# Kernel optimization log

Hardware: AMD Instinct MI355X
Metric: run time of the kernel (lower is better)

The kernel has to match this reference:

```python
import jax, jax.numpy as jnp
import numpy as np

INPUT_BITS = 1024   # window size
N_STATE = 2048      # state-layer neurons
N_OUT = 256         # output-layer neurons
NB_S = 16           # bits per state neuron
NB_O = 16           # bits per output neuron
HASH = 65536        # RAM table size per neuron (2**16 -> hash == direct address)
T = 64              # number of windows (65536 / 1024)


def _addresses(bits, conn, nbits):
    # bits: [n_in] int32 in {0,1}; conn: [N, nbits] int32 indices into bits
    pow2 = (jnp.int32(1) << jnp.arange(nbits, dtype=jnp.int32))  # [nbits]
    gathered = bits[conn]                                        # [N, nbits]
    return (gathered * pow2).sum(axis=-1) % HASH                 # [N]


def setup_inputs() -> dict:
    key = jax.random.key(0)
    k1, k2, k3, k4, k5 = jax.random.split(key, 5)
    input_bits = jax.random.randint(k1, (1, T * INPUT_BITS), 0, 2, dtype=jnp.int32)
    conn_state = jax.random.randint(k2, (N_STATE, NB_S), 0, INPUT_BITS + N_STATE, dtype=jnp.int32)
    conn_out = jax.random.randint(k3, (N_OUT, NB_O), 0, N_STATE, dtype=jnp.int32)
    # RAM lookup tables (learned contents), float so cell values are differentiable
    state_table = jax.random.uniform(k4, (N_STATE, HASH), dtype=jnp.float32)
    output_table = jax.random.uniform(k5, (N_OUT, HASH), dtype=jnp.float32)
    return {
        "input_bits": input_bits,
        "conn_state": conn_state,
        "conn_out": conn_out,
        "state_table": state_table,
        "output_table": output_table,
    }


def reference(input_bits, conn_state, conn_out, state_table, output_table):
    # make_windows: [1, T*INPUT_BITS] -> T windows of [INPUT_BITS]
    windows = input_bits.reshape(T, INPUT_BITS)

    def step(state_bits, window):
        # state_layer_input = cat([window_bits, state_bits])  -> [INPUT_BITS + N_STATE]
        x = jnp.concatenate([window, state_bits])
        addr = _addresses(x, conn_state, NB_S)                           # [N_STATE]
        vals = jnp.take_along_axis(state_table, addr[:, None], axis=1)[:, 0]
        new_state = (vals > 0.5).astype(jnp.int32)  # detach/clone: state is discrete bits
        return new_state, None

    state0 = jnp.zeros((N_STATE,), dtype=jnp.int32)  # _reset_state: all zeros
    final_state, _ = jax.lax.scan(step, state0, windows)

    # output layer on final state (only the last step's output is returned)
    addr = _addresses(final_state, conn_out, NB_O)                       # [N_OUT]
    out = jnp.take_along_axis(output_table, addr[:, None], axis=1)[:, 0]
    return out[None, :]  # [1, N_OUT] raw table reads (decoder thresholds these)
```

## Files before the change

### kernel.cpp

```cpp
#include <hip/hip_runtime.h>

#define T_STEPS 64
#define INPUT_BITS 1024
#define N_STATE 2048
#define N_OUT 256
#define NB 16
#define HASHROW 65536
#define NBLK 32

#define WS_CNT  0
#define WS_BUF0 8
#define WS_BUF1 72
#define WS_PK   192
#define WS_WORDS_NEEDED 2240

__global__ __launch_bounds__(256) void ram_init_kernel(
    const int* __restrict__ input_bits, unsigned int* __restrict__ ws)
{
    const int tid = threadIdx.x, lane = tid & 63;
    const int gw = blockIdx.x * 4 + (tid >> 6);
#pragma unroll
    for (int i = 0; i < 8; i++) {
        int g = gw * 8 + i;
        int v = input_bits[g * 64 + lane];
        unsigned long long m = __ballot(v != 0);
        if (lane == 0) {
            ws[WS_PK + 2 * g]     = (unsigned int)(m & 0xFFFFFFFFull);
            ws[WS_PK + 2 * g + 1] = (unsigned int)(m >> 32);
        }
    }
    if (blockIdx.x == 0 && tid < 192) ws[tid] = 0u;
}

__global__ __launch_bounds__(256) void ram_main_kernel(
    const int* __restrict__ conn_state,
    const int* __restrict__ conn_out,
    const float* __restrict__ state_table,
    const float* __restrict__ output_table,
    unsigned int* __restrict__ ws,
    float* __restrict__ out)
{
    __shared__ unsigned int pk[2048];
    __shared__ unsigned int xw[96];

    const int tid = threadIdx.x, lane = tid & 63, wave = tid >> 6;
    const int b = blockIdx.x;

    for (int i = tid; i < 2048; i += 256) pk[i] = ws[WS_PK + i];

    const unsigned int neuron = (unsigned int)(b * 64 + lane);
    int cn[NB];
#pragma unroll
    for (int j = 0; j < NB; j++) cn[j] = conn_state[neuron * NB + j];
    const float* row = state_table + (size_t)neuron * HASHROW;

    if (wave == 0) xw[32 + lane] = 0u;
    __syncthreads();
    if (wave == 0 && lane < 32) xw[lane] = pk[lane];
    __syncthreads();

    unsigned int* const buf0 = ws + WS_BUF0;
    unsigned int* const buf1 = ws + WS_BUF1;
    unsigned int* const cnt  = ws + WS_CNT;

    for (int t = 0; t < T_STEPS; t++) {
        unsigned int* const bw = ((t + 1) & 1) ? buf1 : buf0;
        if (wave == 0) {
            unsigned int a = 0;
#pragma unroll
            for (int j = 0; j < NB; j++)
                a |= ((xw[cn[j] >> 5] >> (cn[j] & 31)) & 1u) << j;
            float v = row[a];
            unsigned long long m = __ballot(v > 0.5f);
            if (lane == 0) {
                __hip_atomic_store(&bw[2 * b],     (unsigned int)(m & 0xFFFFFFFFull),
                                   __ATOMIC_RELAXED, __HIP_MEMORY_SCOPE_AGENT);
                __hip_atomic_store(&bw[2 * b + 1], (unsigned int)(m >> 32),
                                   __ATOMIC_RELAXED, __HIP_MEMORY_SCOPE_AGENT);
            }
        }
        __syncthreads();
        if (tid == 0) {
            __hip_atomic_fetch_add(cnt, 1u, __ATOMIC_ACQ_REL, __HIP_MEMORY_SCOPE_AGENT);
            const unsigned int target = (unsigned int)(NBLK * (t + 1));
            while (__hip_atomic_load(cnt, __ATOMIC_ACQUIRE, __HIP_MEMORY_SCOPE_AGENT) < target)
                __builtin_amdgcn_s_sleep(1);
        }
        __syncthreads();
        if (wave == 0) {
            unsigned int s = __hip_atomic_load(&bw[lane], __ATOMIC_RELAXED,
                                               __HIP_MEMORY_SCOPE_AGENT);
            xw[32 + lane] = s;
            if (t < T_STEPS - 1 && lane < 32) xw[lane] = pk[(t + 1) * 32 + lane];
        }
        __syncthreads();
    }

    if (b < 4 && wave == 0) {
        const int o = b * 64 + lane;
        unsigned int a = 0;
#pragma unroll
        for (int j = 0; j < NB; j++) {
            int c = conn_out[o * NB + j];
            a |= ((xw[32 + (c >> 5)] >> (c & 31)) & 1u) << j;
        }
        out[o] = output_table[(size_t)o * HASHROW + a];
    }
}

__global__ __launch_bounds__(1024) void ram_seq_kernel(
    const int* __restrict__ input_bits, const int* __restrict__ conn_state,
    const int* __restrict__ conn_out, const float* __restrict__ state_table,
    const float* __restrict__ output_table, float* __restrict__ out)
{
    __shared__ unsigned int pk[2048];
    __shared__ unsigned int xw[96];
    const int tid = threadIdx.x, lane = tid & 63, wave = tid >> 6;

    for (int g = wave; g < 1024; g += 16) {
        int v = input_bits[g * 64 + lane];
        unsigned long long m = __ballot(v != 0);
        if (lane == 0) {
            pk[2 * g] = (unsigned int)(m & 0xFFFFFFFFull);
            pk[2 * g + 1] = (unsigned int)(m >> 32);
        }
    }
    if (tid < 64) xw[32 + tid] = 0u;
    int c0[NB], c1[NB];
#pragma unroll
    for (int j = 0; j < NB; j++) {
        c0[j] = conn_state[tid * NB + j];
        c1[j] = conn_state[(tid + 1024) * NB + j];
    }
    const float* row0 = state_table + (size_t)tid * HASHROW;
    const float* row1 = state_table + (size_t)(tid + 1024) * HASHROW;
    __syncthreads();
    if (tid < 32) xw[tid] = pk[tid];
    __syncthreads();
    for (int t = 0; t < T_STEPS; t++) {
        unsigned int a0 = 0, a1 = 0;
#pragma unroll
        for (int j = 0; j < NB; j++) {
            a0 |= ((xw[c0[j] >> 5] >> (c0[j] & 31)) & 1u) << j;
            a1 |= ((xw[c1[j] >> 5] >> (c1[j] & 31)) & 1u) << j;
        }
        float v0 = row0[a0], v1 = row1[a1];
        __syncthreads();
        unsigned long long m0 = __ballot(v0 > 0.5f);
        unsigned long long m1 = __ballot(v1 > 0.5f);
        if (lane == 0) {
            xw[32 + 2 * wave] = (unsigned int)(m0 & 0xFFFFFFFFull);
            xw[32 + 2 * wave + 1] = (unsigned int)(m0 >> 32);
            xw[64 + 2 * wave] = (unsigned int)(m1 & 0xFFFFFFFFull);
            xw[64 + 2 * wave + 1] = (unsigned int)(m1 >> 32);
        }
        if (t < T_STEPS - 1 && tid < 32) xw[tid] = pk[(t + 1) * 32 + tid];
        __syncthreads();
    }
    if (tid < N_OUT) {
        unsigned int a = 0;
#pragma unroll
        for (int j = 0; j < NB; j++) {
            int c = conn_out[tid * NB + j];
            a |= ((xw[32 + (c >> 5)] >> (c & 31)) & 1u) << j;
        }
        out[tid] = output_table[(size_t)tid * HASHROW + a];
    }
}

extern "C" void kernel_launch(void* const* d_in, const int* in_sizes, int n_in,
                              void* d_out, int out_size, void* d_ws, size_t ws_size,
                              hipStream_t stream) {
    const int*   input_bits   = (const int*)d_in[0];
    const int*   conn_state   = (const int*)d_in[1];
    const int*   conn_out     = (const int*)d_in[2];
    const float* state_table  = (const float*)d_in[3];
    const float* output_table = (const float*)d_in[4];
    float*       out          = (float*)d_out;

    if (ws_size >= WS_WORDS_NEEDED * sizeof(unsigned int)) {
        unsigned int* ws = (unsigned int*)d_ws;
        ram_init_kernel<<<NBLK, 256, 0, stream>>>(input_bits, ws);
        ram_main_kernel<<<NBLK, 256, 0, stream>>>(conn_state, conn_out, state_table,
                                                  output_table, ws, out);
    } else {
        ram_seq_kernel<<<1, 1024, 0, stream>>>(input_bits, conn_state, conn_out,
                                               state_table, output_table, out);
    }
}
```

Before: 805.6 us.

## Replace counter grid barrier with tagged 64-bit flag exchange in single-wave blocks

Replaces the global atomic-counter barrier (fetch_add plus a sleep-polling spin and several __syncthreads per step) with per-block 64-bit slots that pack a step tag alongside each 32-bit state word. Every lane of a single-wave block polls its own slot until the tag matches the current step. Blocks shrink to one wave, which removes the intra-block syncs, and conn_out is preloaded before the loop. This takes the serialized atomic counter and sleep latency off the critical path of each of the 64 steps, at the cost of many lanes spinning on global memory without sleeping.

```diff
diff --git a/kernel.cpp b/kernel.cpp
--- a/kernel.cpp
+++ b/kernel.cpp
@@ -8,11 +8,8 @@
 #define HASHROW 65536
 #define NBLK 32
 
-#define WS_CNT  0
-#define WS_BUF0 8
-#define WS_BUF1 72
-#define WS_PK   192
-#define WS_WORDS_NEEDED 2240
+#define WS_PK 256
+#define WS_WORDS_NEEDED 2304
 
 __global__ __launch_bounds__(256) void ram_init_kernel(
     const int* __restrict__ input_bits, unsigned int* __restrict__ ws)
@@ -29,10 +26,10 @@
             ws[WS_PK + 2 * g + 1] = (unsigned int)(m >> 32);
         }
     }
-    if (blockIdx.x == 0 && tid < 192) ws[tid] = 0u;
+    if (blockIdx.x == 0 && tid < 256) ws[tid] = 0u;
 }
 
-__global__ __launch_bounds__(256) void ram_main_kernel(
+__global__ __launch_bounds__(64) void ram_main_kernel(
     const int* __restrict__ conn_state,
     const int* __restrict__ conn_out,
     const float* __restrict__ state_table,
@@ -43,10 +40,10 @@
     __shared__ unsigned int pk[2048];
     __shared__ unsigned int xw[96];
 
-    const int tid = threadIdx.x, lane = tid & 63, wave = tid >> 6;
+    const int lane = threadIdx.x;
     const int b = blockIdx.x;
 
-    for (int i = tid; i < 2048; i += 256) pk[i] = ws[WS_PK + i];
+    for (int i = lane; i < 2048; i += 64) pk[i] = ws[WS_PK + i];
 
     const unsigned int neuron = (unsigned int)(b * 64 + lane);
     int cn[NB];
@@ -54,57 +51,58 @@
     for (int j = 0; j < NB; j++) cn[j] = conn_state[neuron * NB + j];
     const float* row = state_table + (size_t)neuron * HASHROW;
 
-    if (wave == 0) xw[32 + lane] = 0u;
-    __syncthreads();
-    if (wave == 0 && lane < 32) xw[lane] = pk[lane];
+    int co[NB];
+    if (b < 4) {
+#pragma unroll
+        for (int j = 0; j < NB; j++) co[j] = conn_out[(b * 64 + lane) * NB + j];
+    }
+
+    xw[32 + lane] = 0u;
+    if (lane < 32) xw[lane] = pk[lane];
     __syncthreads();
 
-    unsigned int* const buf0 = ws + WS_BUF0;
-    unsigned int* const buf1 = ws + WS_BUF1;
-    unsigned int* const cnt  = ws + WS_CNT;
+    unsigned long long* const sbuf = (unsigned long long*)ws;
 
     for (int t = 0; t < T_STEPS; t++) {
-        unsigned int* const bw = ((t + 1) & 1) ? buf1 : buf0;
-        if (wave == 0) {
-            unsigned int a = 0;
+        unsigned int a = 0;
 #pragma unroll
-            for (int j = 0; j < NB; j++)
-                a |= ((xw[cn[j] >> 5] >> (cn[j] & 31)) & 1u) << j;
-            float v = row[a];
-            unsigned long long m = __ballot(v > 0.5f);
-            if (lane == 0) {
-                __hip_atomic_store(&bw[2 * b],     (unsigned int)(m & 0xFFFFFFFFull),
-                                   __ATOMIC_RELAXED, __HIP_MEMORY_SCOPE_AGENT);
-                __hip_atomic_store(&bw[2 * b + 1], (unsigned int)(m >> 32),
-                                   __ATOMIC_RELAXED, __HIP_MEMORY_SCOPE_AGENT);
+        for (int j = 0; j < NB; j++)
+            a |= ((xw[cn[j] >> 5] >> (cn[j] & 31)) & 1u) << j;
+        float v = row[a];
+        unsigned long long m = __ballot(v > 0.5f);
+
+        const unsigned int tag = (unsigned int)(t + 1);
+        unsigned long long* const bw = sbuf + (size_t)((t + 1) & 1) * 64;
+
+        if (lane < 2) {
+            unsigned int half = (lane == 0) ? (unsigned int)(m & 0xFFFFFFFFull)
+                                            : (unsigned int)(m >> 32);
+            __hip_atomic_store(&bw[2 * b + lane],
+                               ((unsigned long long)tag << 32) | (unsigned long long)half,
+                               __ATOMIC_RELAXED, __HIP_MEMORY_SCOPE_AGENT);
+        }
+
+        if (t < T_STEPS - 1 && lane < 32) xw[lane] = pk[(t + 1) * 32 + lane];
+
+        unsigned long long vv = 0;
+        bool done = false;
+        for (;;) {
+            if (!done) {
+                vv = __hip_atomic_load(&bw[lane], __ATOMIC_RELAXED,
+                                       __HIP_MEMORY_SCOPE_AGENT);
+                done = ((unsigned int)(vv >> 32) == tag);
             }
+            if (__all(done)) break;
         }
-        __syncthreads();
-        if (tid == 0) {
-            __hip_atomic_fetch_add(cnt, 1u, __ATOMIC_ACQ_REL, __HIP_MEMORY_SCOPE_AGENT);
-            const unsigned int target = (unsigned int)(NBLK * (t + 1));
-            while (__hip_atomic_load(cnt, __ATOMIC_ACQUIRE, __HIP_MEMORY_SCOPE_AGENT) < target)
-                __builtin_amdgcn_s_sleep(1);
-        }
-        __syncthreads();
-        if (wave == 0) {
-            unsigned int s = __hip_atomic_load(&bw[lane], __ATOMIC_RELAXED,
-                                               __HIP_MEMORY_SCOPE_AGENT);
-            xw[32 + lane] = s;
-            if (t < T_STEPS - 1 && lane < 32) xw[lane] = pk[(t + 1) * 32 + lane];
-        }
-        __syncthreads();
+        xw[32 + lane] = (unsigned int)(vv & 0xFFFFFFFFull);
     }
 
-    if (b < 4 && wave == 0) {
-        const int o = b * 64 + lane;
+    if (b < 4) {
         unsigned int a = 0;
 #pragma unroll
-        for (int j = 0; j < NB; j++) {
-            int c = conn_out[o * NB + j];
-            a |= ((xw[32 + (c >> 5)] >> (c & 31)) & 1u) << j;
-        }
-        out[o] = output_table[(size_t)o * HASHROW + a];
+        for (int j = 0; j < NB; j++)
+            a |= ((xw[32 + (co[j] >> 5)] >> (co[j] & 31)) & 1u) << j;
+        out[b * 64 + lane] = output_table[(size_t)(b * 64 + lane) * HASHROW + a];
     }
 }
 
@@ -181,8 +179,8 @@
     if (ws_size >= WS_WORDS_NEEDED * sizeof(unsigned int)) {
         unsigned int* ws = (unsigned int*)d_ws;
         ram_init_kernel<<<NBLK, 256, 0, stream>>>(input_bits, ws);
-        ram_main_kernel<<<NBLK, 256, 0, stream>>>(conn_state, conn_out, state_table,
-                                                  output_table, ws, out);
+        ram_main_kernel<<<NBLK, 64, 0, stream>>>(conn_state, conn_out, state_table,
+                                                 output_table, ws, out);
     } else {
         ram_seq_kernel<<<1, 1024, 0, stream>>>(input_bits, conn_state, conn_out,
                                                state_table, output_table, out);
```

Result: faster. 744.1 us (-7.6%).
